# Performance work log

Hardware: AMD Instinct MI355X
Metric: run time of the kernel (lower is better)

The kernel has to match this reference:

```python
import jax, jax.numpy as jnp
import numpy as np
from jax import lax

BS, CNT, W, P, E, K, L = 32, 128, 2048, 1024, 8, 25, 2


def setup_inputs() -> dict:
    key = jax.random.key(0)
    ks = jax.random.split(key, 12)
    s = lambda k, shape, scale: jax.random.normal(k, shape, dtype=jnp.float32) * scale
    return {
        "x": s(ks[0], (BS, CNT, W), 1.0),
        "conv_w": s(ks[1], (L, E, 1, K), 0.2),
        "conv_b": s(ks[2], (L, E), 0.02),
        "wq": s(ks[3], (L, P, W), 0.02),
        "bq": s(ks[4], (L, P), 0.02),
        "wk": s(ks[5], (L, P, W), 0.02),
        "bk": s(ks[6], (L, P), 0.02),
        "wv": s(ks[7], (L, P, W), 0.02),
        "bv": s(ks[8], (L, P), 0.02),
        "wo": s(ks[9], (L, W, P), 0.02),
        "bo": s(ks[10], (L, W), 0.02),
    }


def _moe(x, w, b):
    # x: [bs, cnt, W]; w: [E, 1, K]; b: [E]
    bs, cnt, d = x.shape
    xf = x.reshape(bs * cnt, 1, d)
    pad = K // 2
    y = lax.conv_general_dilated(
        xf, w, window_strides=(1,), padding=[(pad, pad)],
        dimension_numbers=("NCH", "OIH", "NCH"))  # [bs*cnt, E, W]
    y = y + b[None, :, None]
    return y.mean(axis=1).reshape(bs, cnt, d)


def _fe(x, wq, bq, wk, bk, wv, bv, wo, bo):
    # x: [bs, cnt, W]; projections to P, FFT-domain attention, back to W
    q = jnp.einsum("bcw,pw->bcp", x, wq) + bq
    k = jnp.einsum("bcw,pw->bcp", x, wk) + bk
    v = jnp.einsum("bcw,pw->bcp", x, wv) + bv
    q_fft = jnp.fft.fft(q, axis=-1)
    k_fft = jnp.fft.fft(k, axis=-1)
    v_fft = jnp.fft.fft(v, axis=-1)
    scale = jnp.sqrt(jnp.float32(P))
    weighted = (k_fft * jnp.conj(q_fft)) / scale * v_fft
    wv_real = jnp.fft.ifft(weighted, axis=-1).real.astype(x.dtype)
    return jnp.einsum("bcp,wp->bcw", wv_real, wo) + bo


def reference(x, conv_w, conv_b, wq, bq, wk, bk, wv, bv, wo, bo):
    for l in range(L):
        x = _moe(x, conv_w[l], conv_b[l])
        x = _fe(x, wq[l], bq[l], wk[l], bk[l], wv[l], bv[l], wo[l], bo[l])
    return x
```

## Files before the change

kernel.cpp:

```cpp
#include <hip/hip_runtime.h>
#include <hip/hip_bf16.h>

#define BSZ 32
#define CNTS 128
#define WD 2048
#define PD 1024
#define ED 8
#define KSZ 25
#define LN 2
#define MROWS (BSZ*CNTS)
#define QKVN (3*PD)
#define NWL (PD*WD)

typedef _Float16 f16;
typedef __attribute__((ext_vector_type(8))) _Float16 f16x8;
typedef __attribute__((ext_vector_type(4))) float f32x4;
typedef __attribute__((ext_vector_type(2))) float f32x2;

#define PI_F 3.14159265358979323846f
#define PAD(a) ((a) + ((a) >> 5))

__global__ __launch_bounds__(256) void cvt_layer(
    const float* __restrict__ wq, const float* __restrict__ wk,
    const float* __restrict__ wv, const float* __restrict__ wo,
    f16* __restrict__ wqkv16, f16* __restrict__ wo16)
{
    const int i = (blockIdx.x * 256 + threadIdx.x) * 4;
    const float* src;
    f16* dst;
    if (i < 3*NWL) {
        dst = wqkv16 + i;
        src = (i < NWL) ? wq + i : (i < 2*NWL) ? wk + (i - NWL) : wv + (i - 2*NWL);
    } else {
        dst = wo16 + (i - 3*NWL);
        src = wo + (i - 3*NWL);
    }
    const float4 v = *(const float4*)src;
    f16 o[4];
    o[0] = (f16)v.x; o[1] = (f16)v.y; o[2] = (f16)v.z; o[3] = (f16)v.w;
    *(ushort4*)dst = *(const ushort4*)o;
}

template<typename IT>
__global__ __launch_bounds__(256) void conv_moe(
    const IT* __restrict__ xin,
    const float* __restrict__ cw,
    const float* __restrict__ cb,
    f16* __restrict__ xo)
{
    __shared__ float srow[WD];
    __shared__ float swb[KSZ];
    __shared__ float sbb;
    const int tid = threadIdx.x;
    const size_t row = blockIdx.x;
    if (tid < KSZ) {
        float s = 0.f;
        for (int e = 0; e < ED; ++e) s += cw[e*KSZ + tid];
        swb[tid] = s * (1.f/ED);
    }
    if (tid == 32) {
        float s = 0.f;
        for (int e = 0; e < ED; ++e) s += cb[e];
        sbb = s * (1.f/ED);
    }
    const IT* xr = xin + row*WD;
    if constexpr (sizeof(IT) == 2) {
        const f16x8 v = *(const f16x8*)(xr + tid*8);
        #pragma unroll
        for (int j = 0; j < 8; ++j) srow[tid*8 + j] = (float)v[j];
    } else {
        const float4 v0 = *(const float4*)(xr + tid*8);
        const float4 v1 = *(const float4*)(xr + tid*8 + 4);
        srow[tid*8+0] = v0.x; srow[tid*8+1] = v0.y; srow[tid*8+2] = v0.z; srow[tid*8+3] = v0.w;
        srow[tid*8+4] = v1.x; srow[tid*8+5] = v1.y; srow[tid*8+6] = v1.z; srow[tid*8+7] = v1.w;
    }
    __syncthreads();
    const float bb = sbb;
    float w[32];
    #pragma unroll
    for (int k = 0; k < 32; ++k) {
        const int idx = tid*8 + k - (KSZ/2);
        w[k] = (idx >= 0 && idx < WD) ? srow[idx] : 0.f;
    }
    f16 o[8];
    #pragma unroll
    for (int j = 0; j < 8; ++j) {
        float acc = bb;
        #pragma unroll
        for (int k = 0; k < KSZ; ++k) acc = fmaf(w[j+k], swb[k], acc);
        o[j] = (f16)acc;
    }
    *(f16x8*)(xo + row*WD + tid*8) = *(const f16x8*)o;
}

__global__ __launch_bounds__(512, 2) void gemm192(
    const f16* __restrict__ A,
    const f16* __restrict__ B,
    const float* __restrict__ c0, const float* __restrict__ c1, const float* __restrict__ c2,
    f16* __restrict__ out,
    const int K, const int N)
{
    __shared__ __align__(16) f16 sA[2][2][128*64];
    __shared__ __align__(16) f16 sB[2][3][64*64];

    const int tid  = threadIdx.x;
    const int lane = tid & 63;
    const int wave = tid >> 6;
    const int wr   = wave >> 2;
    const int wc   = wave & 3;
    const int quad = lane >> 4;
    const int r16  = lane & 15;
    const int xrA  = r16 & 7;

    const int orig = blockIdx.x;
    const int xcd  = orig & 7;
    const int loc  = orig >> 3;
    const int mt   = (xcd >> 1) * 4 + (loc & 3);
    const int nt   = (xcd & 1) * 8 + (loc >> 2);
    const int m0   = mt * 256;
    const int n0   = nt * 192;

    f32x4 acc[8][3] = {};
    f16x8 bf[3][2];
    f16x8 aX0, aX1, aX2, aX3, aY0, aY1, aY2, aY3, aZ0, aZ1, aZ2, aZ3;

    int soffA[2];
    #pragma unroll
    for (int t = 0; t < 2; ++t) {
        const int s = tid + 512*t;
        const int row = s >> 3;
        soffA[t] = row * K + (((s & 7) ^ (row & 7)) * 8);
    }
    int soffB;
    {
        const int row = tid >> 3;
        soffB = row * K + (((tid & 7) ^ (row & 7)) * 8);
    }

    int bPiece[3], bBase[3], bXor[3];
    #pragma unroll
    for (int j = 0; j < 3; ++j) {
        const int rb = wc*48 + j*16 + r16;
        bPiece[j] = rb >> 6;
        bBase[j]  = (rb & 63) << 3;
        bXor[j]   = rb & 7;
    }

    const f16* Abase[2] = { A + (size_t)m0 * K, A + (size_t)(m0 + 128) * K };
    const f16* Bp[3]    = { B + (size_t)n0 * K, B + (size_t)(n0 + 64) * K,
                            B + (size_t)(n0 + 128) * K };

    #define STAGE_A(BUF, HALF, GOFF)                                              \
      { _Pragma("unroll") for (int t = 0; t < 2; ++t) {                           \
          __builtin_amdgcn_global_load_lds(                                       \
            (const __attribute__((address_space(1))) unsigned int*)(Abase[HALF] + soffA[t] + (GOFF)), \
            (__attribute__((address_space(3))) unsigned int*)&sA[BUF][HALF][(tid + 512*t)*8], \
            16, 0, 0); } }

    #define STAGE_B(BUF, PIECE, GOFF)                                             \
      { __builtin_amdgcn_global_load_lds(                                         \
          (const __attribute__((address_space(1))) unsigned int*)(Bp[PIECE] + soffB + (GOFF)), \
          (__attribute__((address_space(3))) unsigned int*)&sB[BUF][PIECE][tid*8], \
          16, 0, 0); }

    #define LDA(BUF, ROW, C) \
      (*(const f16x8*)&sA[BUF][wr][ (((ROW) << 3) + ((C) ^ xrA)) * 8 ])

    #define LDB(BUF, J, C) \
      (*(const f16x8*)&sB[BUF][bPiece[J]][ (bBase[J] + ((C) ^ bXor[J])) * 8 ])

    #define READ_BF(BUF)                                                          \
      { _Pragma("unroll") for (int j = 0; j < 3; ++j) {                           \
          bf[j][0] = LDB(BUF, j, quad);                                           \
          bf[j][1] = LDB(BUF, j, 4 + quad);                                       \
        } }

    #define READ_A(BUF, Q, D0, D1, D2, D3)                                        \
      D0 = LDA(BUF, (2*(Q))*16   + r16, quad);                                    \
      D1 = LDA(BUF, (2*(Q))*16   + r16, 4 + quad);                                \
      D2 = LDA(BUF, (2*(Q)+1)*16 + r16, quad);                                    \
      D3 = LDA(BUF, (2*(Q)+1)*16 + r16, 4 + quad);

    #define MFMA_Q(Q, D0, D1, D2, D3)                                             \
      __builtin_amdgcn_s_setprio(1);                                              \
      { _Pragma("unroll") for (int jj = 0; jj < 3; ++jj) {                        \
          acc[2*(Q)][jj]   = __builtin_amdgcn_mfma_f32_16x16x32_f16(D0, bf[jj][0], acc[2*(Q)][jj],   0,0,0); \
          acc[2*(Q)+1][jj] = __builtin_amdgcn_mfma_f32_16x16x32_f16(D2, bf[jj][0], acc[2*(Q)+1][jj], 0,0,0); \
        } }                                                                       \
      { _Pragma("unroll") for (int jj = 0; jj < 3; ++jj) {                        \
          acc[2*(Q)][jj]   = __builtin_amdgcn_mfma_f32_16x16x32_f16(D1, bf[jj][1], acc[2*(Q)][jj],   0,0,0); \
          acc[2*(Q)+1][jj] = __builtin_amdgcn_mfma_f32_16x16x32_f16(D3, bf[jj][1], acc[2*(Q)+1][jj], 0,0,0); \
        } }                                                                       \
      __builtin_amdgcn_s_setprio(0);

    #define LGKM(n) asm volatile("s_waitcnt lgkmcnt(" #n ")" ::: "memory");       \
                    __builtin_amdgcn_sched_barrier(0);
    #define VMC(n)  asm volatile("s_waitcnt vmcnt(" #n ")" ::: "memory");
    #define BAR()   __builtin_amdgcn_s_barrier();

    STAGE_B(0, 0, 0); STAGE_B(0, 1, 0); STAGE_B(0, 2, 0);
    STAGE_A(0, 0, 0); STAGE_A(0, 1, 0);
    STAGE_B(1, 0, 64); STAGE_B(1, 1, 64); STAGE_B(1, 2, 64);
    VMC(3)
    BAR()

    const int NIT = K >> 7;
    for (int it = 0; it < NIT; ++it) {
        const bool kl = (it == NIT - 1);
        const int kb1 = (2*it + 1) * 64;
        const int kb2 = kb1 + 64;
        const int kb3 = kb1 + 128;

        STAGE_A(1, 0, kb1);
        READ_BF(0)
        READ_A(0, 0, aX0, aX1, aX2, aX3)
        LGKM(0)
        MFMA_Q(0, aX0, aX1, aX2, aX3)
        BAR()
        STAGE_A(1, 1, kb1);
        READ_A(0, 1, aY0, aY1, aY2, aY3)
        READ_A(0, 2, aZ0, aZ1, aZ2, aZ3)
        LGKM(4)
        MFMA_Q(1, aY0, aY1, aY2, aY3)
        if (!kl) { STAGE_B(0, 0, kb2); STAGE_B(0, 1, kb2); }
        READ_A(0, 3, aX0, aX1, aX2, aX3)
        LGKM(4)
        MFMA_Q(2, aZ0, aZ1, aZ2, aZ3)
        if (!kl) { STAGE_B(0, 2, kb2); }
        LGKM(0)
        MFMA_Q(3, aX0, aX1, aX2, aX3)
        if (!kl) { VMC(3) } else { VMC(0) }
        BAR()

        if (!kl) STAGE_A(0, 0, kb2);
        READ_BF(1)
        READ_A(1, 0, aX0, aX1, aX2, aX3)
        LGKM(0)
        MFMA_Q(0, aX0, aX1, aX2, aX3)
        BAR()
        if (!kl) STAGE_A(0, 1, kb2);
        READ_A(1, 1, aY0, aY1, aY2, aY3)
        READ_A(1, 2, aZ0, aZ1, aZ2, aZ3)
        LGKM(4)
        MFMA_Q(1, aY0, aY1, aY2, aY3)
        if (!kl) { STAGE_B(1, 0, kb3); STAGE_B(1, 1, kb3); }
        READ_A(1, 3, aX0, aX1, aX2, aX3)
        LGKM(4)
        MFMA_Q(2, aZ0, aZ1, aZ2, aZ3)
        if (!kl) { STAGE_B(1, 2, kb3); }
        LGKM(0)
        MFMA_Q(3, aX0, aX1, aX2, aX3)
        if (!kl) { VMC(3) }
        BAR()
    }

    #pragma unroll
    for (int j = 0; j < 3; ++j) {
        const int col = n0 + wc*48 + j*16 + r16;
        const float bv = (col < 1024) ? c0[col] : (col < 2048) ? c1[col-1024] : c2[col-2048];
        #pragma unroll
        for (int mi = 0; mi < 8; ++mi) {
            #pragma unroll
            for (int r = 0; r < 4; ++r) {
                const int rowg = m0 + wr*128 + mi*16 + quad*4 + r;
                out[(size_t)rowg*N + col] = (f16)(acc[mi][j][r] + bv);
            }
        }
    }

    #undef STAGE_A
    #undef STAGE_B
    #undef LDA
    #undef LDB
    #undef READ_BF
    #undef READ_A
    #undef MFMA_Q
    #undef LGKM
    #undef VMC
    #undef BAR
}

template<typename OT>
__global__ __launch_bounds__(512, 2) void gemmOP(
    const f16* __restrict__ A,
    const f16* __restrict__ B,
    const float* __restrict__ c0, const float* __restrict__ c1,
    OT* __restrict__ out,
    const int K, const int N)
{
    __shared__ __align__(16) f16 sA[2][2][128*64];
    __shared__ __align__(16) f16 sB[2][2][64*64];

    const int tid  = threadIdx.x;
    const int lane = tid & 63;
    const int wave = tid >> 6;
    const int wr   = wave >> 2;
    const int wc   = wave & 3;
    const int quad = lane >> 4;
    const int r16  = lane & 15;
    const int xrA  = r16 & 7;

    const int orig = blockIdx.x;
    const int xcd  = orig & 7;
    const int loc  = orig >> 3;
    const int mt   = (xcd >> 1) * 4 + (loc & 3);
    const int nt   = (xcd & 1) * 8 + (loc >> 2);
    const int m0   = mt * 256;
    const int n0   = nt * 128;

    f32x4 acc[8][2] = {};
    f16x8 bf[2][2];
    f16x8 aX0, aX1, aX2, aX3, aY0, aY1, aY2, aY3, aZ0, aZ1, aZ2, aZ3;

    int soffA[2];
    #pragma unroll
    for (int t = 0; t < 2; ++t) {
        const int s = tid + 512*t;
        const int row = s >> 3;
        soffA[t] = row * K + (((s & 7) ^ (row & 7)) * 8);
    }
    int soffB;
    {
        const int row = tid >> 3;
        soffB = row * K + (((tid & 7) ^ (row & 7)) * 8);
    }

    int bPiece[2], bBase[2], bXor[2];
    #pragma unroll
    for (int j = 0; j < 2; ++j) {
        const int rb = wc*32 + j*16 + r16;
        bPiece[j] = rb >> 6;
        bBase[j]  = (rb & 63) << 3;
        bXor[j]   = rb & 7;
    }

    const f16* Abase[2] = { A + (size_t)m0 * K, A + (size_t)(m0 + 128) * K };
    const f16* Bp[2]    = { B + (size_t)n0 * K, B + (size_t)(n0 + 64) * K };

    #define STAGE_A(BUF, HALF, GOFF)                                              \
      { _Pragma("unroll") for (int t = 0; t < 2; ++t) {                           \
          __builtin_amdgcn_global_load_lds(                                       \
            (const __attribute__((address_space(1))) unsigned int*)(Abase[HALF] + soffA[t] + (GOFF)), \
            (__attribute__((address_space(3))) unsigned int*)&sA[BUF][HALF][(tid + 512*t)*8], \
            16, 0, 0); } }

    #define STAGE_B(BUF, PIECE, GOFF)                                             \
      { __builtin_amdgcn_global_load_lds(                                         \
          (const __attribute__((address_space(1))) unsigned int*)(Bp[PIECE] + soffB + (GOFF)), \
          (__attribute__((address_space(3))) unsigned int*)&sB[BUF][PIECE][tid*8], \
          16, 0, 0); }

    #define LDA(BUF, ROW, C) \
      (*(const f16x8*)&sA[BUF][wr][ (((ROW) << 3) + ((C) ^ xrA)) * 8 ])

    #define LDB(BUF, J, C) \
      (*(const f16x8*)&sB[BUF][bPiece[J]][ (bBase[J] + ((C) ^ bXor[J])) * 8 ])

    #define READ_BF(BUF)                                                          \
      { _Pragma("unroll") for (int j = 0; j < 2; ++j) {                           \
          bf[j][0] = LDB(BUF, j, quad);                                           \
          bf[j][1] = LDB(BUF, j, 4 + quad);                                       \
        } }

    #define READ_A(BUF, Q, D0, D1, D2, D3)                                        \
      D0 = LDA(BUF, (2*(Q))*16   + r16, quad);                                    \
      D1 = LDA(BUF, (2*(Q))*16   + r16, 4 + quad);                                \
      D2 = LDA(BUF, (2*(Q)+1)*16 + r16, quad);                                    \
      D3 = LDA(BUF, (2*(Q)+1)*16 + r16, 4 + quad);

    #define MFMA_Q(Q, D0, D1, D2, D3)                                             \
      __builtin_amdgcn_s_setprio(1);                                              \
      { _Pragma("unroll") for (int jj = 0; jj < 2; ++jj) {                        \
          acc[2*(Q)][jj]   = __builtin_amdgcn_mfma_f32_16x16x32_f16(D0, bf[jj][0], acc[2*(Q)][jj],   0,0,0); \
          acc[2*(Q)+1][jj] = __builtin_amdgcn_mfma_f32_16x16x32_f16(D2, bf[jj][0], acc[2*(Q)+1][jj], 0,0,0); \
        } }                                                                       \
      { _Pragma("unroll") for (int jj = 0; jj < 2; ++jj) {                        \
          acc[2*(Q)][jj]   = __builtin_amdgcn_mfma_f32_16x16x32_f16(D1, bf[jj][1], acc[2*(Q)][jj],   0,0,0); \
          acc[2*(Q)+1][jj] = __builtin_amdgcn_mfma_f32_16x16x32_f16(D3, bf[jj][1], acc[2*(Q)+1][jj], 0,0,0); \
        } }                                                                       \
      __builtin_amdgcn_s_setprio(0);

    #define LGKM(n) asm volatile("s_waitcnt lgkmcnt(" #n ")" ::: "memory");       \
                    __builtin_amdgcn_sched_barrier(0);
    #define VMC(n)  asm volatile("s_waitcnt vmcnt(" #n ")" ::: "memory");
    #define BAR()   __builtin_amdgcn_s_barrier();

    STAGE_B(0, 0, 0); STAGE_B(0, 1, 0);
    STAGE_A(0, 0, 0); STAGE_A(0, 1, 0);
    STAGE_B(1, 0, 64); STAGE_B(1, 1, 64);
    VMC(2)
    BAR()

    const int NIT = K >> 7;
    for (int it = 0; it < NIT; ++it) {
        const bool kl = (it == NIT - 1);
        const int kb1 = (2*it + 1) * 64;
        const int kb2 = kb1 + 64;
        const int kb3 = kb1 + 128;

        STAGE_A(1, 0, kb1);
        READ_BF(0)
        READ_A(0, 0, aX0, aX1, aX2, aX3)
        LGKM(0)
        MFMA_Q(0, aX0, aX1, aX2, aX3)
        BAR()
        STAGE_A(1, 1, kb1);
        READ_A(0, 1, aY0, aY1, aY2, aY3)
        READ_A(0, 2, aZ0, aZ1, aZ2, aZ3)
        LGKM(4)
        MFMA_Q(1, aY0, aY1, aY2, aY3)
        if (!kl) { STAGE_B(0, 0, kb2); }
        READ_A(0, 3, aX0, aX1, aX2, aX3)
        LGKM(4)
        MFMA_Q(2, aZ0, aZ1, aZ2, aZ3)
        if (!kl) { STAGE_B(0, 1, kb2); }
        LGKM(0)
        MFMA_Q(3, aX0, aX1, aX2, aX3)
        if (!kl) { VMC(2) } else { VMC(0) }
        BAR()

        if (!kl) STAGE_A(0, 0, kb2);
        READ_BF(1)
        READ_A(1, 0, aX0, aX1, aX2, aX3)
        LGKM(0)
        MFMA_Q(0, aX0, aX1, aX2, aX3)
        BAR()
        if (!kl) STAGE_A(0, 1, kb2);
        READ_A(1, 1, aY0, aY1, aY2, aY3)
        READ_A(1, 2, aZ0, aZ1, aZ2, aZ3)
        LGKM(4)
        MFMA_Q(1, aY0, aY1, aY2, aY3)
        if (!kl) { STAGE_B(1, 0, kb3); }
        READ_A(1, 3, aX0, aX1, aX2, aX3)
        LGKM(4)
        MFMA_Q(2, aZ0, aZ1, aZ2, aZ3)
        if (!kl) { STAGE_B(1, 1, kb3); }
        LGKM(0)
        MFMA_Q(3, aX0, aX1, aX2, aX3)
        if (!kl) { VMC(2) }
        BAR()
    }

    #pragma unroll
    for (int j = 0; j < 2; ++j) {
        const int col = n0 + wc*32 + j*16 + r16;
        const float bv = (col < 1024) ? c0[col] : c1[col-1024];
        #pragma unroll
        for (int mi = 0; mi < 8; ++mi) {
            #pragma unroll
            for (int r = 0; r < 4; ++r) {
                const int rowg = m0 + wr*128 + mi*16 + quad*4 + r;
                out[(size_t)rowg*N + col] = (OT)(acc[mi][j][r] + bv);
            }
        }
    }

    #undef STAGE_A
    #undef STAGE_B
    #undef LDA
    #undef LDB
    #undef READ_BF
    #undef READ_A
    #undef MFMA_Q
    #undef LGKM
    #undef VMC
    #undef BAR
}

__device__ inline void fft1024r4(f32x2* x, f32x2* y, const int tid,
                                 const float* tws, const float* twc)
{
    f32x2* src = x;
    f32x2* dst = y;
    #pragma unroll
    for (int st = 0; st < 5; ++st) {
        const int ls = 2*st;
        const int s  = 1 << ls;
        const int p  = tid >> ls;
        const int q  = tid & (s - 1);
        const f32x2 a = src[PAD(tid)];
        const f32x2 b = src[PAD(tid + 256)];
        const f32x2 c = src[PAD(tid + 512)];
        const f32x2 d = src[PAD(tid + 768)];
        const float ws = tws[st], wc = twc[st];
        const float apcx = a.x + c.x, apcy = a.y + c.y;
        const float amcx = a.x - c.x, amcy = a.y - c.y;
        const float bpdx = b.x + d.x, bpdy = b.y + d.y;
        const float bmdx = b.x - d.x, bmdy = b.y - d.y;
        f32x2 y0; y0.x = apcx + bpdx; y0.y = apcy + bpdy;
        const float t1x = amcx + bmdy, t1y = amcy - bmdx;
        const float t2x = apcx - bpdx, t2y = apcy - bpdy;
        const float t3x = amcx - bmdy, t3y = amcy + bmdx;
        const float w2x = wc*wc - ws*ws, w2y = 2.f*wc*ws;
        const float w3x = w2x*wc - w2y*ws, w3y = w2x*ws + w2y*wc;
        f32x2 y1; y1.x = wc*t1x - ws*t1y;   y1.y = wc*t1y + ws*t1x;
        f32x2 y2; y2.x = w2x*t2x - w2y*t2y; y2.y = w2x*t2y + w2y*t2x;
        f32x2 y3; y3.x = w3x*t3x - w3y*t3y; y3.y = w3x*t3y + w3y*t3x;
        const int base = q + ((p * s) << 2);
        dst[PAD(base)]       = y0;
        dst[PAD(base + s)]   = y1;
        dst[PAD(base + 2*s)] = y2;
        dst[PAD(base + 3*s)] = y3;
        __syncthreads();
        f32x2* t = src; src = dst; dst = t;
    }
}

__global__ __launch_bounds__(256) void fft_attn2(
    const f16* __restrict__ qkv, f16* __restrict__ outg)
{
    __shared__ f32x2 X[PAD(1023)+1], Y[PAD(1023)+1];
    __shared__ f16 st[2*QKVN];
    const int tid = threadIdx.x;
    const size_t row0 = (size_t)blockIdx.x * 2;
    const f16* r1 = qkv + row0*QKVN;
    const f16* r2 = r1 + QKVN;

    #pragma unroll
    for (int p = 0; p < 3; ++p) {
        const int c = tid + 256*p;
        const f16* src = (c < 384) ? (r1 + (c)*8) : (r2 + (c - 384)*8);
        *(f16x8*)&st[c*8] = *(const f16x8*)src;
    }

    float tws[5], twc[5];
    #pragma unroll
    for (int s5 = 0; s5 < 5; ++s5) {
        const int ls = 2*s5;
        const int p  = tid >> ls;
        __sincosf(-2.f*PI_F * (float)p / (float)(1024 >> ls), &tws[s5], &twc[s5]);
    }
    __syncthreads();

    const f16* s1 = st;
    const f16* s2 = st + QKVN;

    f32x2 V1[4], V2[4], S1[4], S2[4];

    #pragma unroll
    for (int k = 0; k < 4; ++k) {
        const int i = tid + 256*k;
        f32x2 t; t.x = (float)s1[2048+i]; t.y = (float)s2[2048+i];
        X[PAD(i)] = t;
    }
    __syncthreads();
    fft1024r4(X, Y, tid, tws, twc);
    #pragma unroll
    for (int k = 0; k < 4; ++k) {
        const int f = tid + 256*k;
        const int g = (PD - f) & (PD-1);
        const f32x2 z1 = Y[PAD(f)], z2 = Y[PAD(g)];
        V1[k].x = 0.5f*(z1.x + z2.x); V1[k].y = 0.5f*(z1.y - z2.y);
        V2[k].x = 0.5f*(z1.y + z2.y); V2[k].y = 0.5f*(z2.x - z1.x);
    }

    #pragma unroll
    for (int k = 0; k < 4; ++k) {
        const int i = tid + 256*k;
        f32x2 t; t.x = (float)s1[i]; t.y = (float)s1[1024+i];
        X[PAD(i)] = t;
    }
    __syncthreads();
    fft1024r4(X, Y, tid, tws, twc);
    #pragma unroll
    for (int k = 0; k < 4; ++k) {
        const int f = tid + 256*k;
        const int g = (PD - f) & (PD-1);
        const f32x2 z1 = Y[PAD(f)], z2 = Y[PAD(g)];
        const float Qr = 0.5f*(z1.x + z2.x), Qi = 0.5f*(z1.y - z2.y);
        const float Kr = 0.5f*(z1.y + z2.y), Ki = 0.5f*(z2.x - z1.x);
        const float Pr = (Kr*Qr + Ki*Qi) * (1.f/32.f);
        const float Pi = (Ki*Qr - Kr*Qi) * (1.f/32.f);
        S1[k].x = Pr*V1[k].x - Pi*V1[k].y;
        S1[k].y = -(Pr*V1[k].y + Pi*V1[k].x);
    }

    #pragma unroll
    for (int k = 0; k < 4; ++k) {
        const int i = tid + 256*k;
        f32x2 t; t.x = (float)s2[i]; t.y = (float)s2[1024+i];
        X[PAD(i)] = t;
    }
    __syncthreads();
    fft1024r4(X, Y, tid, tws, twc);
    #pragma unroll
    for (int k = 0; k < 4; ++k) {
        const int f = tid + 256*k;
        const int g = (PD - f) & (PD-1);
        const f32x2 z1 = Y[PAD(f)], z2 = Y[PAD(g)];
        const float Qr = 0.5f*(z1.x + z2.x), Qi = 0.5f*(z1.y - z2.y);
        const float Kr = 0.5f*(z1.y + z2.y), Ki = 0.5f*(z2.x - z1.x);
        const float Pr = (Kr*Qr + Ki*Qi) * (1.f/32.f);
        const float Pi = (Ki*Qr - Kr*Qi) * (1.f/32.f);
        S2[k].x = Pr*V2[k].x - Pi*V2[k].y;
        S2[k].y = -(Pr*V2[k].y + Pi*V2[k].x);
    }

    #pragma unroll
    for (int k = 0; k < 4; ++k) {
        const int f = tid + 256*k;
        f32x2 t; t.x = S1[k].x - S2[k].y; t.y = S1[k].y + S2[k].x;
        X[PAD(f)] = t;
    }
    __syncthreads();
    fft1024r4(X, Y, tid, tws, twc);
    f16* o1 = outg + row0*PD;
    f16* o2 = o1 + PD;
    #pragma unroll
    for (int k = 0; k < 4; ++k) {
        const int n = tid + 256*k;
        const f32x2 z = Y[PAD(n)];
        o1[n] = (f16)(z.x * (1.f/1024.f));
        o2[n] = (f16)(z.y * (1.f/1024.f));
    }
}

extern "C" void kernel_launch(void* const* d_in, const int* in_sizes, int n_in,
                              void* d_out, int out_size, void* d_ws, size_t ws_size,
                              hipStream_t stream)
{
    const float* x      = (const float*)d_in[0];
    const float* conv_w = (const float*)d_in[1];
    const float* conv_b = (const float*)d_in[2];
    const float* wq     = (const float*)d_in[3];
    const float* bq     = (const float*)d_in[4];
    const float* wk     = (const float*)d_in[5];
    const float* bk     = (const float*)d_in[6];
    const float* wv     = (const float*)d_in[7];
    const float* bv     = (const float*)d_in[8];
    const float* wo     = (const float*)d_in[9];
    const float* bo     = (const float*)d_in[10];

    char* ws = (char*)d_ws;
    const size_t MB = 1024*1024;
    f16*   wqkv16 = (f16*)(ws);
    f16*   wo16   = (f16*)(ws + 12*MB);
    f16*   qkvbuf = (f16*)(ws + 16*MB);
    f16*   xc16   = (f16*)(ws + 40*MB);
    f16*   xmid   = (f16*)(ws + 56*MB);
    f16*   wvr16  = xc16;

    for (int l = 0; l < LN; ++l) {
        cvt_layer<<<dim3(4*NWL/4/256), dim3(256), 0, stream>>>(
            wq + (size_t)l*NWL, wk + (size_t)l*NWL, wv + (size_t)l*NWL, wo + (size_t)l*NWL,
            wqkv16, wo16);

        if (l == 0)
            conv_moe<float><<<dim3(MROWS), dim3(256), 0, stream>>>(
                x, conv_w, conv_b, xc16);
        else
            conv_moe<f16><<<dim3(MROWS), dim3(256), 0, stream>>>(
                xmid, conv_w + (size_t)l*ED*KSZ, conv_b + (size_t)l*ED, xc16);

        gemm192<<<dim3((MROWS/256)*(QKVN/192)), dim3(512), 0, stream>>>(
            xc16, wqkv16,
            bq + (size_t)l*PD, bk + (size_t)l*PD, bv + (size_t)l*PD,
            qkvbuf, WD, QKVN);

        fft_attn2<<<dim3(MROWS/2), dim3(256), 0, stream>>>(qkvbuf, wvr16);

        if (l == LN-1)
            gemmOP<float><<<dim3((MROWS/256)*(WD/128)), dim3(512), 0, stream>>>(
                wvr16, wo16,
                bo + (size_t)l*WD, bo + (size_t)l*WD + PD,
                (float*)d_out, PD, WD);
        else
            gemmOP<f16><<<dim3((MROWS/256)*(WD/128)), dim3(512), 0, stream>>>(
                wvr16, wo16,
                bo + (size_t)l*WD, bo + (size_t)l*WD + PD,
                xmid, PD, WD);
    }
}
```

Before: 411.9 us.

## Rewrite FFT attention as wave-per-row-pair register FFT without block barriers

```diff
diff --git a/kernel.cpp b/kernel.cpp
--- a/kernel.cpp
+++ b/kernel.cpp
@@ -18,7 +18,6 @@
 typedef __attribute__((ext_vector_type(2))) float f32x2;
 
 #define PI_F 3.14159265358979323846f
-#define PAD(a) ((a) + ((a) >> 5))
 
 __global__ __launch_bounds__(256) void cvt_layer(
     const float* __restrict__ wq, const float* __restrict__ wk,
@@ -467,152 +466,271 @@
     #undef BAR
 }
 
-__device__ inline void fft1024r4(f32x2* x, f32x2* y, const int tid,
-                                 const float* tws, const float* twc)
-{
-    f32x2* src = x;
-    f32x2* dst = y;
-    #pragma unroll
-    for (int st = 0; st < 5; ++st) {
-        const int ls = 2*st;
-        const int s  = 1 << ls;
-        const int p  = tid >> ls;
-        const int q  = tid & (s - 1);
-        const f32x2 a = src[PAD(tid)];
-        const f32x2 b = src[PAD(tid + 256)];
-        const f32x2 c = src[PAD(tid + 512)];
-        const f32x2 d = src[PAD(tid + 768)];
-        const float ws = tws[st], wc = twc[st];
-        const float apcx = a.x + c.x, apcy = a.y + c.y;
-        const float amcx = a.x - c.x, amcy = a.y - c.y;
-        const float bpdx = b.x + d.x, bpdy = b.y + d.y;
-        const float bmdx = b.x - d.x, bmdy = b.y - d.y;
-        f32x2 y0; y0.x = apcx + bpdx; y0.y = apcy + bpdy;
-        const float t1x = amcx + bmdy, t1y = amcy - bmdx;
-        const float t2x = apcx - bpdx, t2y = apcy - bpdy;
-        const float t3x = amcx - bmdy, t3y = amcy + bmdx;
-        const float w2x = wc*wc - ws*ws, w2y = 2.f*wc*ws;
-        const float w3x = w2x*wc - w2y*ws, w3y = w2x*ws + w2y*wc;
-        f32x2 y1; y1.x = wc*t1x - ws*t1y;   y1.y = wc*t1y + ws*t1x;
-        f32x2 y2; y2.x = w2x*t2x - w2y*t2y; y2.y = w2x*t2y + w2y*t2x;
-        f32x2 y3; y3.x = w3x*t3x - w3y*t3y; y3.y = w3x*t3y + w3y*t3x;
-        const int base = q + ((p * s) << 2);
-        dst[PAD(base)]       = y0;
-        dst[PAD(base + s)]   = y1;
-        dst[PAD(base + 2*s)] = y2;
-        dst[PAD(base + 3*s)] = y3;
-        __syncthreads();
-        f32x2* t = src; src = dst; dst = t;
-    }
+__device__ __forceinline__ f32x2 cmul2(const f32x2 a, const float wc, const float ws) {
+    f32x2 r; r.x = a.x*wc - a.y*ws; r.y = a.y*wc + a.x*ws; return r;
 }
 
-__global__ __launch_bounds__(256) void fft_attn2(
+#define IZ(c,i) ((c)*65 + ((i) ^ ((((i) >> 4) & 3) << 2)))
+#define WSYNC() { asm volatile("s_waitcnt lgkmcnt(0)" ::: "memory"); \
+                  __builtin_amdgcn_sched_barrier(0); }
+
+__global__ __launch_bounds__(256) void fft_attn_wave(
     const f16* __restrict__ qkv, f16* __restrict__ outg)
 {
-    __shared__ f32x2 X[PAD(1023)+1], Y[PAD(1023)+1];
-    __shared__ f16 st[2*QKVN];
+    __shared__ f32x2 ZZ[4][2][16*65];
     const int tid = threadIdx.x;
-    const size_t row0 = (size_t)blockIdx.x * 2;
-    const f16* r1 = qkv + row0*QKVN;
+    const int w   = tid >> 6;
+    const int l   = tid & 63;
+    const int t   = l & 15;
+    const int cg  = l >> 4;
+    f32x2* Z1 = &ZZ[w][0][0];
+    f32x2* Z2 = &ZZ[w][1][0];
+    f16*   sc = (f16*)Z1;
+
+    const size_t rp = (size_t)blockIdx.x*4 + w;
+    const f16* r1 = qkv + (2*rp)*QKVN;
     const f16* r2 = r1 + QKVN;
 
-    #pragma unroll
-    for (int p = 0; p < 3; ++p) {
-        const int c = tid + 256*p;
-        const f16* src = (c < 384) ? (r1 + (c)*8) : (r2 + (c - 384)*8);
-        *(f16x8*)&st[c*8] = *(const f16x8*)src;
-    }
-
-    float tws[5], twc[5];
-    #pragma unroll
-    for (int s5 = 0; s5 < 5; ++s5) {
-        const int ls = 2*s5;
-        const int p  = tid >> ls;
-        __sincosf(-2.f*PI_F * (float)p / (float)(1024 >> ls), &tws[s5], &twc[s5]);
-    }
-    __syncthreads();
-
-    const f16* s1 = st;
-    const f16* s2 = st + QKVN;
-
-    f32x2 V1[4], V2[4], S1[4], S2[4];
-
-    #pragma unroll
-    for (int k = 0; k < 4; ++k) {
-        const int i = tid + 256*k;
-        f32x2 t; t.x = (float)s1[2048+i]; t.y = (float)s2[2048+i];
-        X[PAD(i)] = t;
-    }
-    __syncthreads();
-    fft1024r4(X, Y, tid, tws, twc);
-    #pragma unroll
-    for (int k = 0; k < 4; ++k) {
-        const int f = tid + 256*k;
-        const int g = (PD - f) & (PD-1);
-        const f32x2 z1 = Y[PAD(f)], z2 = Y[PAD(g)];
-        V1[k].x = 0.5f*(z1.x + z2.x); V1[k].y = 0.5f*(z1.y - z2.y);
-        V2[k].x = 0.5f*(z1.y + z2.y); V2[k].y = 0.5f*(z2.x - z1.x);
-    }
-
-    #pragma unroll
-    for (int k = 0; k < 4; ++k) {
-        const int i = tid + 256*k;
-        f32x2 t; t.x = (float)s1[i]; t.y = (float)s1[1024+i];
-        X[PAD(i)] = t;
-    }
-    __syncthreads();
-    fft1024r4(X, Y, tid, tws, twc);
-    #pragma unroll
-    for (int k = 0; k < 4; ++k) {
-        const int f = tid + 256*k;
-        const int g = (PD - f) & (PD-1);
-        const f32x2 z1 = Y[PAD(f)], z2 = Y[PAD(g)];
+    float bwc[16], bws[16];
+    {
+        const float th = -2.f*PI_F*(float)l*(1.f/1024.f);
+        bwc[0]=1.f; bws[0]=0.f;
+        __sincosf(th,     &bws[1], &bwc[1]);
+        __sincosf(2.f*th, &bws[2], &bwc[2]);
+        __sincosf(4.f*th, &bws[4], &bwc[4]);
+        __sincosf(8.f*th, &bws[8], &bwc[8]);
+        bwc[3]=bwc[1]*bwc[2]-bws[1]*bws[2]; bws[3]=bws[1]*bwc[2]+bwc[1]*bws[2];
+        bwc[5]=bwc[1]*bwc[4]-bws[1]*bws[4]; bws[5]=bws[1]*bwc[4]+bwc[1]*bws[4];
+        bwc[6]=bwc[2]*bwc[4]-bws[2]*bws[4]; bws[6]=bws[2]*bwc[4]+bwc[2]*bws[4];
+        bwc[7]=bwc[3]*bwc[4]-bws[3]*bws[4]; bws[7]=bws[3]*bwc[4]+bwc[3]*bws[4];
+        #pragma unroll
+        for (int k = 9; k < 16; ++k) {
+            bwc[k]=bwc[k-8]*bwc[8]-bws[k-8]*bws[8];
+            bws[k]=bws[k-8]*bwc[8]+bwc[k-8]*bws[8];
+        }
+    }
+    float c0s, c0c, c1s, c1c;
+    __sincosf(-2.f*PI_F*(float)t*(1.f/64.f), &c0s, &c0c);
+    __sincosf(-2.f*PI_F*(float)(t>>2)*(1.f/16.f), &c1s, &c1c);
+
+    const float W16C[10] = {1.f, 0.92387953f, 0.70710678f, 0.38268343f, 0.f,
+                            0.f, -0.70710678f, 0.f, 0.f, -0.92387953f};
+    const float W16S[10] = {0.f, -0.38268343f, -0.70710678f, -0.92387953f, -1.f,
+                            0.f, -0.70710678f, 0.f, 0.f, 0.38268343f};
+
+    f32x2 v[16], V1[16], V2[16];
+
+    auto run_fft = [&]() {
+        f32x2 C[4][4];
+        #pragma unroll
+        for (int jj = 0; jj < 4; ++jj) {
+            const f32x2 a = v[jj], b = v[jj+4], c = v[jj+8], d = v[jj+12];
+            f32x2 t0, t1, t2, t3;
+            t0.x=a.x+c.x; t0.y=a.y+c.y; t1.x=a.x-c.x; t1.y=a.y-c.y;
+            t2.x=b.x+d.x; t2.y=b.y+d.y; t3.x=b.x-d.x; t3.y=b.y-d.y;
+            f32x2 B0, B1, B2, B3;
+            B0.x=t0.x+t2.x; B0.y=t0.y+t2.y;
+            B1.x=t1.x+t3.y; B1.y=t1.y-t3.x;
+            B2.x=t0.x-t2.x; B2.y=t0.y-t2.y;
+            B3.x=t1.x-t3.y; B3.y=t1.y+t3.x;
+            C[0][jj] = B0;
+            C[1][jj] = cmul2(B1, W16C[jj],   W16S[jj]);
+            C[2][jj] = cmul2(B2, W16C[2*jj], W16S[2*jj]);
+            C[3][jj] = cmul2(B3, W16C[3*jj], W16S[3*jj]);
+        }
+        f32x2 g[16];
+        #pragma unroll
+        for (int q = 0; q < 4; ++q) {
+            const f32x2 c0 = C[q][0], c1 = C[q][1], c2 = C[q][2], c3 = C[q][3];
+            f32x2 e0, o0, e1, o1;
+            e0.x=c0.x+c2.x; e0.y=c0.y+c2.y; o0.x=c1.x+c3.x; o0.y=c1.y+c3.y;
+            e1.x=c0.x-c2.x; e1.y=c0.y-c2.y; o1.x=c1.x-c3.x; o1.y=c1.y-c3.y;
+            g[q].x    = e0.x+o0.x; g[q].y    = e0.y+o0.y;
+            g[q+4].x  = e1.x+o1.y; g[q+4].y  = e1.y-o1.x;
+            g[q+8].x  = e0.x-o0.x; g[q+8].y  = e0.y-o0.y;
+            g[q+12].x = e1.x-o1.y; g[q+12].y = e1.y+o1.x;
+        }
+        WSYNC()
+        #pragma unroll
+        for (int k = 0; k < 16; ++k)
+            Z1[IZ(k, l)] = cmul2(g[k], bwc[k], bws[k]);
+        WSYNC()
+        #pragma unroll
+        for (int pass = 0; pass < 4; ++pass) {
+            const int c = cg + 4*pass;
+            const f32x2 a = Z1[IZ(c, t)],     b = Z1[IZ(c, t+16)];
+            const f32x2 cc = Z1[IZ(c, t+32)], d = Z1[IZ(c, t+48)];
+            const float apcx=a.x+cc.x, apcy=a.y+cc.y, amcx=a.x-cc.x, amcy=a.y-cc.y;
+            const float bpdx=b.x+d.x,  bpdy=b.y+d.y,  bmdx=b.x-d.x,  bmdy=b.y-d.y;
+            f32x2 y0; y0.x=apcx+bpdx; y0.y=apcy+bpdy;
+            const float t1x=amcx+bmdy, t1y=amcy-bmdx;
+            const float t2x=apcx-bpdx, t2y=apcy-bpdy;
+            const float t3x=amcx-bmdy, t3y=amcy+bmdx;
+            const float w2x=c0c*c0c-c0s*c0s, w2y=2.f*c0c*c0s;
+            const float w3x=w2x*c0c-w2y*c0s, w3y=w2x*c0s+w2y*c0c;
+            f32x2 y1; y1.x=c0c*t1x-c0s*t1y; y1.y=c0c*t1y+c0s*t1x;
+            f32x2 y2; y2.x=w2x*t2x-w2y*t2y; y2.y=w2x*t2y+w2y*t2x;
+            f32x2 y3; y3.x=w3x*t3x-w3y*t3y; y3.y=w3x*t3y+w3y*t3x;
+            const int i0 = 4*t;
+            Z2[IZ(c, i0)]   = y0; Z2[IZ(c, i0+1)] = y1;
+            Z2[IZ(c, i0+2)] = y2; Z2[IZ(c, i0+3)] = y3;
+        }
+        WSYNC()
+        #pragma unroll
+        for (int pass = 0; pass < 4; ++pass) {
+            const int c = cg + 4*pass;
+            const f32x2 a = Z2[IZ(c, t)],     b = Z2[IZ(c, t+16)];
+            const f32x2 cc = Z2[IZ(c, t+32)], d = Z2[IZ(c, t+48)];
+            const float apcx=a.x+cc.x, apcy=a.y+cc.y, amcx=a.x-cc.x, amcy=a.y-cc.y;
+            const float bpdx=b.x+d.x,  bpdy=b.y+d.y,  bmdx=b.x-d.x,  bmdy=b.y-d.y;
+            f32x2 y0; y0.x=apcx+bpdx; y0.y=apcy+bpdy;
+            const float t1x=amcx+bmdy, t1y=amcy-bmdx;
+            const float t2x=apcx-bpdx, t2y=apcy-bpdy;
+            const float t3x=amcx-bmdy, t3y=amcy+bmdx;
+            const float w2x=c1c*c1c-c1s*c1s, w2y=2.f*c1c*c1s;
+            const float w3x=w2x*c1c-w2y*c1s, w3y=w2x*c1s+w2y*c1c;
+            f32x2 y1; y1.x=c1c*t1x-c1s*t1y; y1.y=c1c*t1y+c1s*t1x;
+            f32x2 y2; y2.x=w2x*t2x-w2y*t2y; y2.y=w2x*t2y+w2y*t2x;
+            f32x2 y3; y3.x=w3x*t3x-w3y*t3y; y3.y=w3x*t3y+w3y*t3x;
+            const int i0 = (t & 3) + 16*(t >> 2);
+            Z1[IZ(c, i0)]    = y0; Z1[IZ(c, i0+4)]  = y1;
+            Z1[IZ(c, i0+8)]  = y2; Z1[IZ(c, i0+12)] = y3;
+        }
+        WSYNC()
+        #pragma unroll
+        for (int pass = 0; pass < 4; ++pass) {
+            const int c = cg + 4*pass;
+            const f32x2 a = Z1[IZ(c, t)],     b = Z1[IZ(c, t+16)];
+            const f32x2 cc = Z1[IZ(c, t+32)], d = Z1[IZ(c, t+48)];
+            const float apcx=a.x+cc.x, apcy=a.y+cc.y, amcx=a.x-cc.x, amcy=a.y-cc.y;
+            const float bpdx=b.x+d.x,  bpdy=b.y+d.y,  bmdx=b.x-d.x,  bmdy=b.y-d.y;
+            f32x2 y0; y0.x=apcx+bpdx; y0.y=apcy+bpdy;
+            f32x2 y1; y1.x=amcx+bmdy; y1.y=amcy-bmdx;
+            f32x2 y2; y2.x=apcx-bpdx; y2.y=apcy-bpdy;
+            f32x2 y3; y3.x=amcx-bmdy; y3.y=amcy+bmdx;
+            Z2[IZ(c, t)]    = y0; Z2[IZ(c, t+16)] = y1;
+            Z2[IZ(c, t+32)] = y2; Z2[IZ(c, t+48)] = y3;
+        }
+        WSYNC()
+    };
+
+    auto stage2 = [&](const f16* a, const f16* b) {
+        const f16x8 a0 = *(const f16x8*)(a + l*8);
+        const f16x8 a1 = *(const f16x8*)(a + (l+64)*8);
+        const f16x8 b0 = *(const f16x8*)(b + l*8);
+        const f16x8 b1 = *(const f16x8*)(b + (l+64)*8);
+        WSYNC()
+        *(f16x8*)&sc[l*8]          = a0;
+        *(f16x8*)&sc[(l+64)*8]     = a1;
+        *(f16x8*)&sc[1024+l*8]     = b0;
+        *(f16x8*)&sc[1024+(l+64)*8]= b1;
+        WSYNC()
+    };
+
+    stage2(r1 + 2048, r2 + 2048);
+    #pragma unroll
+    for (int j = 0; j < 16; ++j) {
+        v[j].x = (float)sc[l + 64*j];
+        v[j].y = (float)sc[1024 + l + 64*j];
+    }
+    run_fft();
+    #pragma unroll
+    for (int j = 0; j < 16; ++j) {
+        const int f = l + 64*j;
+        const int gg = (PD - f) & (PD-1);
+        const f32x2 z1 = Z2[IZ(f & 15, f >> 4)];
+        const f32x2 z2 = Z2[IZ(gg & 15, gg >> 4)];
+        V1[j].x = 0.5f*(z1.x + z2.x); V1[j].y = 0.5f*(z1.y - z2.y);
+        V2[j].x = 0.5f*(z1.y + z2.y); V2[j].y = 0.5f*(z2.x - z1.x);
+    }
+
+    {
+        const f16x8 a0 = *(const f16x8*)(r1 + l*8);
+        const f16x8 a1 = *(const f16x8*)(r1 + (l+64)*8);
+        const f16x8 a2 = *(const f16x8*)(r1 + (l+128)*8);
+        const f16x8 a3 = *(const f16x8*)(r1 + (l+192)*8);
+        WSYNC()
+        *(f16x8*)&sc[l*8]        = a0;
+        *(f16x8*)&sc[(l+64)*8]   = a1;
+        *(f16x8*)&sc[(l+128)*8]  = a2;
+        *(f16x8*)&sc[(l+192)*8]  = a3;
+        WSYNC()
+    }
+    #pragma unroll
+    for (int j = 0; j < 16; ++j) {
+        v[j].x = (float)sc[l + 64*j];
+        v[j].y = (float)sc[1024 + l + 64*j];
+    }
+    run_fft();
+    #pragma unroll
+    for (int j = 0; j < 16; ++j) {
+        const int f = l + 64*j;
+        const int gg = (PD - f) & (PD-1);
+        const f32x2 z1 = Z2[IZ(f & 15, f >> 4)];
+        const f32x2 z2 = Z2[IZ(gg & 15, gg >> 4)];
         const float Qr = 0.5f*(z1.x + z2.x), Qi = 0.5f*(z1.y - z2.y);
         const float Kr = 0.5f*(z1.y + z2.y), Ki = 0.5f*(z2.x - z1.x);
         const float Pr = (Kr*Qr + Ki*Qi) * (1.f/32.f);
         const float Pi = (Ki*Qr - Kr*Qi) * (1.f/32.f);
-        S1[k].x = Pr*V1[k].x - Pi*V1[k].y;
-        S1[k].y = -(Pr*V1[k].y + Pi*V1[k].x);
-    }
-
-    #pragma unroll
-    for (int k = 0; k < 4; ++k) {
-        const int i = tid + 256*k;
-        f32x2 t; t.x = (float)s2[i]; t.y = (float)s2[1024+i];
-        X[PAD(i)] = t;
-    }
-    __syncthreads();
-    fft1024r4(X, Y, tid, tws, twc);
-    #pragma unroll
-    for (int k = 0; k < 4; ++k) {
-        const int f = tid + 256*k;
-        const int g = (PD - f) & (PD-1);
-        const f32x2 z1 = Y[PAD(f)], z2 = Y[PAD(g)];
+        const float sx = Pr*V1[j].x - Pi*V1[j].y;
+        const float sy = -(Pr*V1[j].y + Pi*V1[j].x);
+        V1[j].x = sx; V1[j].y = sy;
+    }
+
+    {
+        const f16x8 a0 = *(const f16x8*)(r2 + l*8);
+        const f16x8 a1 = *(const f16x8*)(r2 + (l+64)*8);
+        const f16x8 a2 = *(const f16x8*)(r2 + (l+128)*8);
+        const f16x8 a3 = *(const f16x8*)(r2 + (l+192)*8);
+        WSYNC()
+        *(f16x8*)&sc[l*8]        = a0;
+        *(f16x8*)&sc[(l+64)*8]   = a1;
+        *(f16x8*)&sc[(l+128)*8]  = a2;
+        *(f16x8*)&sc[(l+192)*8]  = a3;
+        WSYNC()
+    }
+    #pragma unroll
+    for (int j = 0; j < 16; ++j) {
+        v[j].x = (float)sc[l + 64*j];
+        v[j].y = (float)sc[1024 + l + 64*j];
+    }
+    run_fft();
+    #pragma unroll
+    for (int j = 0; j < 16; ++j) {
+        const int f = l + 64*j;
+        const int gg = (PD - f) & (PD-1);
+        const f32x2 z1 = Z2[IZ(f & 15, f >> 4)];
+        const f32x2 z2 = Z2[IZ(gg & 15, gg >> 4)];
         const float Qr = 0.5f*(z1.x + z2.x), Qi = 0.5f*(z1.y - z2.y);
         const float Kr = 0.5f*(z1.y + z2.y), Ki = 0.5f*(z2.x - z1.x);
         const float Pr = (Kr*Qr + Ki*Qi) * (1.f/32.f);
         const float Pi = (Ki*Qr - Kr*Qi) * (1.f/32.f);
-        S2[k].x = Pr*V2[k].x - Pi*V2[k].y;
-        S2[k].y = -(Pr*V2[k].y + Pi*V2[k].x);
-    }
-
-    #pragma unroll
-    for (int k = 0; k < 4; ++k) {
-        const int f = tid + 256*k;
-        f32x2 t; t.x = S1[k].x - S2[k].y; t.y = S1[k].y + S2[k].x;
-        X[PAD(f)] = t;
-    }
-    __syncthreads();
-    fft1024r4(X, Y, tid, tws, twc);
-    f16* o1 = outg + row0*PD;
+        const float sx = Pr*V2[j].x - Pi*V2[j].y;
+        const float sy = -(Pr*V2[j].y + Pi*V2[j].x);
+        V2[j].x = sx; V2[j].y = sy;
+    }
+
+    #pragma unroll
+    for (int j = 0; j < 16; ++j) {
+        v[j].x = V1[j].x - V2[j].y;
+        v[j].y = V1[j].y + V2[j].x;
+    }
+    run_fft();
+
+    #pragma unroll
+    for (int j = 0; j < 16; ++j) {
+        const int n = l + 64*j;
+        const f32x2 z = Z2[IZ(n & 15, n >> 4)];
+        sc[n]        = (f16)(z.x * (1.f/1024.f));
+        sc[1024 + n] = (f16)(z.y * (1.f/1024.f));
+    }
+    WSYNC()
+    f16* o1 = outg + (2*rp)*PD;
     f16* o2 = o1 + PD;
-    #pragma unroll
-    for (int k = 0; k < 4; ++k) {
-        const int n = tid + 256*k;
-        const f32x2 z = Y[PAD(n)];
-        o1[n] = (f16)(z.x * (1.f/1024.f));
-        o2[n] = (f16)(z.y * (1.f/1024.f));
-    }
+    *(f16x8*)(o1 + l*8)      = *(const f16x8*)&sc[l*8];
+    *(f16x8*)(o1 + (l+64)*8) = *(const f16x8*)&sc[(l+64)*8];
+    *(f16x8*)(o2 + l*8)      = *(const f16x8*)&sc[1024 + l*8];
+    *(f16x8*)(o2 + (l+64)*8) = *(const f16x8*)&sc[1024 + (l+64)*8];
 }
 
 extern "C" void kernel_launch(void* const* d_in, const int* in_sizes, int n_in,
@@ -657,7 +775,7 @@
             bq + (size_t)l*PD, bk + (size_t)l*PD, bv + (size_t)l*PD,
             qkvbuf, WD, QKVN);
 
-        fft_attn2<<<dim3(MROWS/2), dim3(256), 0, stream>>>(qkvbuf, wvr16);
+        fft_attn_wave<<<dim3(MROWS/8), dim3(256), 0, stream>>>(qkvbuf, wvr16);
 
         if (l == LN-1)
             gemmOP<float><<<dim3((MROWS/256)*(WD/128)), dim3(512), 0, stream>>>(
```

Measured after the change: 427.0 us. 1.04x slower.
